# Performance work log

Measured on AMD Instinct MI355X. Metric: run time of the kernel, lower is better.

The kernel has to match this reference:

```python
import jax, jax.numpy as jnp
import numpy as np

K_CLS, M_PROTO, C = 19, 10, 720
EPS_SK, SK_ITERS = 0.05, 3  # standard distributed_sinkhorn defaults (SwAV/ProtoSeg)


def _layernorm(x, g, b, eps=1e-5):
    mu = jnp.mean(x, axis=-1, keepdims=True)
    var = jnp.var(x, axis=-1, keepdims=True)
    return (x - mu) * jax.lax.rsqrt(var + eps) * g + b


def _l2n(x):
    return x / jnp.clip(jnp.linalg.norm(x, axis=-1, keepdims=True), 1e-12, None)


def _masked_sinkhorn(scores, mask):
    # scores: [K, N, M] per-class similarity; mask: [K, N] (1.0 where gt_seg == class k)
    # Faithful to distributed_sinkhorn(init_q) run per class, vectorized over classes
    # with masking instead of data-dependent boolean gather (jit-safe).
    L = jnp.exp(scores / EPS_SK) * mask[..., None]                     # [K, N, M]
    L = L / jnp.clip(jnp.sum(L, axis=(1, 2), keepdims=True), 1e-12, None)
    n = jnp.sum(mask, axis=1)[:, None, None]                           # pixels per class [K,1,1]
    n_safe = jnp.maximum(n, 1.0)

    def body(L, _):
        # normalize each prototype row (sum over pixels), then divide by M
        L = L / jnp.clip(jnp.sum(L, axis=1, keepdims=True), 1e-12, None) / M_PROTO
        # normalize each pixel column (sum over prototypes), then divide by n
        L = L / jnp.clip(jnp.sum(L, axis=2, keepdims=True), 1e-12, None) / n_safe
        L = L * mask[..., None]
        return L, None

    L, _ = jax.lax.scan(body, L, None, length=SK_ITERS)
    return L * n_safe                                                  # [K, N, M]


def setup_inputs() -> dict:
    key = jax.random.key(0)
    k1, k2, k3 = jax.random.split(key, 3)
    N = 4 * 128 * 128  # batch 4, 512x512 crop at HRNet output stride 4
    return {
        "x": jax.random.normal(k1, (N, C), jnp.float32),
        "gt_seg": jax.random.randint(k2, (N,), 0, K_CLS),
        "feat_gamma": jnp.ones((C,), jnp.float32),
        "feat_beta": jnp.zeros((C,), jnp.float32),
        "prototypes": jax.random.normal(k3, (K_CLS, M_PROTO, C), jnp.float32) * 0.02,
    }


def reference(x, gt_seg, feat_gamma, feat_beta, prototypes):
    # similarity_compute (cosine branch)
    xn = _l2n(_layernorm(x, feat_gamma, feat_beta))                    # [N, C]
    protos = _l2n(prototypes)                                          # [K, M, C]
    sim_mat = jnp.einsum('nd,kmd->nmk', xn, protos)                    # [N, M, K]

    # prototype_learning
    s = jnp.max(sim_mat, axis=1)                                       # amax over prototypes -> [N, K]
    pred_seg = jnp.argmax(s, axis=-1)                                  # [N]
    scores = jnp.transpose(sim_mat, (2, 0, 1))                         # [K, N, M]
    mask = jnp.transpose(jax.nn.one_hot(gt_seg, K_CLS, dtype=sim_mat.dtype))  # [K, N]
    q = _masked_sinkhorn(scores, mask)                                 # [K, N, M]
    return sim_mat, q, pred_seg
```

## Files before the change

### kernel.cpp

```cpp
#include <hip/hip_runtime.h>
#include <stdint.h>

#define N_PIX    65536
#define C_DIM    720
#define K_CLS    19
#define M_PROTO  10
#define NPROTO   190
#define CPAD     768
#define OFF_Q    12451840
#define OFF_PRED 24903680

typedef _Float16 half8 __attribute__((ext_vector_type(8)));
typedef float    f32x4 __attribute__((ext_vector_type(4)));

#define WS_E       0u
#define WS_G2      768u
#define WS_G3      1536u
#define WS_CNT     2304u
#define WS_TIECNT  2432u
#define WS_V       2560u
#define WS_PSCALE  4096u
#define WS_EPIX    1052672u
#define WS_U       3674112u
#define WS_TIELIST 3936256u
#define WS_PF16    4198400u
#define WS_PF32    4493312u

__global__ void zero_acc(float* ws) {
    if (threadIdx.x < 640) ws[threadIdx.x] = 0.f;
}

__global__ void proto_prep(const float* __restrict__ protos,
                           _Float16* __restrict__ pf16,
                           float* __restrict__ pf32) {
    int p = blockIdx.x;
    int tid = threadIdx.x;
    if (p >= NPROTO) {
        for (int c = tid; c < CPAD; c += 256) pf16[(size_t)p * CPAD + c] = (_Float16)0.f;
        return;
    }
    __shared__ float red[256];
    const float* row = protos + (size_t)p * C_DIM;
    float ss = 0.f;
    for (int c = tid; c < C_DIM; c += 256) { float v = row[c]; ss += v * v; }
    red[tid] = ss;
    __syncthreads();
    for (int s = 128; s > 0; s >>= 1) {
        if (tid < s) red[tid] += red[tid + s];
        __syncthreads();
    }
    float invn = 1.f / fmaxf(sqrtf(red[0]), 1e-12f);
    for (int c = tid; c < CPAD; c += 256) {
        float v = (c < C_DIM) ? row[c] * invn : 0.f;
        pf16[(size_t)p * CPAD + c] = (_Float16)v;
        if (c < C_DIM) pf32[(size_t)p * C_DIM + c] = v;
    }
}

__global__ void stats_kernel(const float* __restrict__ x,
                             const float* __restrict__ gamma,
                             const float* __restrict__ beta,
                             float4* __restrict__ pscale) {
    int wave = threadIdx.x >> 6, lane = threadIdx.x & 63;
    int n = blockIdx.x * 4 + wave;
    const float* row = x + (size_t)n * C_DIM;
    float a[8];
    #pragma unroll
    for (int t = 0; t < 8; ++t) a[t] = 0.f;
    #pragma unroll
    for (int j = 0; j < 12; ++j) {
        int i = lane + 64 * j;
        if (i < C_DIM) {
            float v = row[i], g = gamma[i], b = beta[i];
            float g2 = g * g;
            a[0] += v;          a[1] += v * v;
            a[2] += v * g2;     a[3] += v * v * g2;
            a[4] += v * g * b;  a[5] += g2;
            a[6] += g * b;      a[7] += b * b;
        }
    }
    #pragma unroll
    for (int m = 1; m < 64; m <<= 1) {
        #pragma unroll
        for (int t = 0; t < 8; ++t) a[t] += __shfl_xor(a[t], m);
    }
    if (lane == 0) {
        float mu   = a[0] * (1.f / 720.f);
        float var  = a[1] * (1.f / 720.f) - mu * mu;
        float rsig = rsqrtf(var + 1e-5f);
        float ny2  = rsig * rsig * (a[3] - 2.f * mu * a[2] + mu * mu * a[5])
                   + 2.f * rsig * (a[4] - mu * a[6]) + a[7];
        float rn   = 1.f / fmaxf(sqrtf(fmaxf(ny2, 0.f)), 1e-12f);
        float pp   = rsig * rn;
        pscale[n]  = make_float4(pp, -pp * mu, rn, 0.f);
    }
}

__global__ __launch_bounds__(256) void gemm_sim(
        const float*  __restrict__ x,
        const float4* __restrict__ pscale,
        const float*  __restrict__ gamma,
        const float*  __restrict__ beta,
        const _Float16* __restrict__ pf16,
        const int*    __restrict__ gt_seg,
        float* __restrict__ out_sim,
        float* __restrict__ out_pred,
        float* __restrict__ epix,
        float* __restrict__ E,
        float* __restrict__ cnt,
        int*   __restrict__ tiecnt,
        int*   __restrict__ tielist) {
    __shared__ __align__(16) char smem[36864];
    _Float16* xs = (_Float16*)smem;
    _Float16* ps = (_Float16*)(smem + 9216);

    int tid = threadIdx.x;
    int wave = tid >> 6, lane = tid & 63;
    int lane15 = lane & 15, quad = lane >> 4;
    int n0 = blockIdx.x * 64;

    f32x4 acc[12];
    #pragma unroll
    for (int ct = 0; ct < 12; ++ct)
        acc[ct] = (f32x4){0.f, 0.f, 0.f, 0.f};

    #pragma unroll 1
    for (int ch = 0; ch < 12; ++ch) {
        __syncthreads();
        int kb4 = ch * 16;
        #pragma unroll
        for (int i = 0; i < 4; ++i) {
            int idx = tid + 256 * i;
            int r = idx >> 4, c4 = idx & 15;
            int gc4 = kb4 + c4;
            float4 xv = make_float4(0.f, 0.f, 0.f, 0.f);
            float4 gv = xv, bv = xv;
            if (gc4 < 180) {
                xv = *(const float4*)(x + (size_t)(n0 + r) * C_DIM + gc4 * 4);
                gv = *(const float4*)(gamma + gc4 * 4);
                bv = *(const float4*)(beta + gc4 * 4);
            }
            float4 sc = pscale[n0 + r];
            union { _Float16 h[4]; uint2 u; } cv;
            cv.h[0] = (_Float16)((sc.x * xv.x + sc.y) * gv.x + sc.z * bv.x);
            cv.h[1] = (_Float16)((sc.x * xv.y + sc.y) * gv.y + sc.z * bv.y);
            cv.h[2] = (_Float16)((sc.x * xv.z + sc.y) * gv.z + sc.z * bv.z);
            cv.h[3] = (_Float16)((sc.x * xv.w + sc.y) * gv.w + sc.z * bv.w);
            *reinterpret_cast<uint2*>(&xs[r * 72 + c4 * 4]) = cv.u;
        }
        #pragma unroll
        for (int i = 0; i < 6; ++i) {
            int idx = tid + 256 * i;
            int r = idx >> 3, c8 = idx & 7;
            int4 v = *(const int4*)(pf16 + (size_t)r * CPAD + ch * 64 + c8 * 8);
            *reinterpret_cast<int4*>(&ps[r * 72 + c8 * 8]) = v;
        }
        __syncthreads();
        #pragma unroll
        for (int ks = 0; ks < 2; ++ks) {
            int col = ks * 32 + quad * 8;
            half8 a0 = *reinterpret_cast<const half8*>(&xs[(wave * 16 + lane15) * 72 + col]);
            half8 b[12];
            #pragma unroll
            for (int ct = 0; ct < 12; ++ct)
                b[ct] = *reinterpret_cast<const half8*>(&ps[(ct * 16 + lane15) * 72 + col]);
            #pragma unroll
            for (int ct = 0; ct < 12; ++ct)
                acc[ct] = __builtin_amdgcn_mfma_f32_16x16x32_f16(a0, b[ct], acc[ct], 0, 0, 0);
        }
    }

    __syncthreads();
    float* fsm   = (float*)smem;
    float* ebuf  = fsm + wave * 1600;
    float* smaxw = fsm + 6400 + wave * 152;
    float* Eks   = fsm + 7008;
    float* hists = fsm + 7200;
    if (tid < 212) fsm[7008 + tid] = 0.f;
    __syncthreads();

    #pragma unroll
    for (int h = 0; h < 2; ++h) {
        if ((quad >> 1) == h) {
            int prow = (quad - 2 * h) * 4;
            #pragma unroll
            for (int ct = 0; ct < 12; ++ct) {
                int proto = ct * 16 + lane15;
                if (proto < NPROTO) {
                    int kc = proto / 10;
                    int m = proto - kc * 10;
                    int obase = m * 19 + kc;
                    #pragma unroll
                    for (int r = 0; r < 4; ++r)
                        ebuf[(prow + r) * 200 + obase] = acc[ct][r];
                }
            }
        }
        __syncthreads();
        #pragma unroll
        for (int p = 0; p < 8; ++p) {
            int pixel = n0 + wave * 16 + 8 * h + p;
            #pragma unroll
            for (int j = 0; j < 3; ++j) {
                int col = lane + 64 * j;
                if (col < NPROTO)
                    out_sim[(size_t)pixel * 190 + col] = ebuf[p * 200 + col];
            }
        }
        #pragma unroll
        for (int t = lane; t < 152; t += 64) {
            int p = t / 19, k = t - p * 19;
            const float* row = ebuf + p * 200;
            float mx = row[k];
            #pragma unroll
            for (int m = 1; m < 10; ++m) mx = fmaxf(mx, row[m * 19 + k]);
            smaxw[t] = mx;
        }
        __syncthreads();
        if (lane < 8) {
            int p = lane;
            int pixel = n0 + wave * 16 + 8 * h + p;
            float best = smaxw[p * 19], second = -1e30f;
            int bk = 0;
            #pragma unroll
            for (int k = 1; k < 19; ++k) {
                float v = smaxw[p * 19 + k];
                if (v > best) { second = best; best = v; bk = k; }
                else if (v > second) second = v;
            }
            out_pred[pixel] = (float)bk;
            if (best - second < 3e-4f) {
                int pos = atomicAdd(tiecnt, 1);
                if (pos < N_PIX) tielist[pos] = pixel;
            }
            int g = gt_seg[pixel];
            atomicAdd(&hists[g], 1.f);
            const float* row = ebuf + p * 200;
            #pragma unroll
            for (int m = 0; m < 10; ++m) {
                float ev = __expf(row[m * 19 + g] * 20.f);
                epix[(size_t)pixel * 10 + m] = ev;
                atomicAdd(&Eks[g * 10 + m], ev);
            }
        }
        __syncthreads();
    }
    if (tid < 190) atomicAdd(&E[tid], Eks[tid]);
    if (tid < 19)  atomicAdd(&cnt[tid], hists[tid]);
}

__global__ void tiefix(const float* __restrict__ x,
                       const float4* __restrict__ pscale,
                       const float* __restrict__ gamma,
                       const float* __restrict__ beta,
                       const float* __restrict__ pf32,
                       const int* __restrict__ tiecnt,
                       const int* __restrict__ tielist,
                       float* __restrict__ out_pred) {
    __shared__ float xrow[720];
    __shared__ double sd[190];
    int count = *tiecnt;
    if (count > N_PIX) count = N_PIX;
    int wave = threadIdx.x >> 6, lane = threadIdx.x & 63;
    for (int it = blockIdx.x; it < count; it += gridDim.x) {
        int n = tielist[it];
        float4 sc = pscale[n];
        for (int c = threadIdx.x; c < 720; c += 256)
            xrow[c] = (sc.x * x[(size_t)n * 720 + c] + sc.y) * gamma[c] + sc.z * beta[c];
        __syncthreads();
        for (int p = wave; p < NPROTO; p += 4) {
            const float* pr = pf32 + (size_t)p * 720;
            double a = 0.0;
            for (int j = 0; j < 12; ++j) {
                int i = lane + 64 * j;
                if (i < 720) a += (double)xrow[i] * (double)pr[i];
            }
            #pragma unroll
            for (int m = 1; m < 64; m <<= 1) a += __shfl_xor(a, m);
            if (lane == 0) sd[p] = a;
        }
        __syncthreads();
        if (threadIdx.x == 0) {
            double best = -1e300;
            int bk = 0;
            for (int k = 0; k < 19; ++k) {
                double sk = -1e300;
                for (int m = 0; m < 10; ++m) sk = fmax(sk, sd[k * 10 + m]);
                if (sk > best) { best = sk; bk = k; }
            }
            out_pred[n] = (float)bk;
        }
        __syncthreads();
    }
}

__global__ void v1k(const float* __restrict__ E, float* __restrict__ v) {
    __shared__ float Es[192];
    int t = threadIdx.x;
    if (t < 192) Es[t] = (t < 190) ? E[t] : 0.f;
    __syncthreads();
    if (t < 190) {
        int k = t / 10;
        float S = 0.f;
        #pragma unroll
        for (int m = 0; m < 10; ++m) S += Es[k * 10 + m];
        float v0 = 1.f / fmaxf(S, 1e-12f);
        float r = v0 * Es[t];
        v[t] = v0 / (fmaxf(r, 1e-12f) * 10.f);
    }
}

__global__ void v23k(float* __restrict__ v, const float* __restrict__ G) {
    int t = threadIdx.x;
    if (t < 190) {
        float r = v[t] * G[t];
        v[t] = v[t] / (fmaxf(r, 1e-12f) * 10.f);
    }
}

__global__ void pk(const float* __restrict__ epix,
                   const int* __restrict__ gt_seg,
                   const float* __restrict__ v,
                   const float* __restrict__ cnt,
                   const float* __restrict__ uin,
                   float* __restrict__ uout,
                   float* __restrict__ G) {
    __shared__ float vs[190];
    __shared__ float cs[19];
    __shared__ float Ga[190];
    int tid = threadIdx.x;
    if (tid < 190) { vs[tid] = v[tid]; Ga[tid] = 0.f; }
    if (tid < 19) cs[tid] = cnt[tid];
    __syncthreads();
    int n = blockIdx.x * 256 + tid;
    int g = gt_seg[n];
    float ns = fmaxf(cs[g], 1.f);
    const float* e = epix + (size_t)n * 10;
    float ev[10];
    float dot = 0.f;
    #pragma unroll
    for (int m = 0; m < 10; ++m) { ev[m] = e[m]; dot += ev[m] * vs[g * 10 + m]; }
    float up = uin ? uin[n] : 1.f;
    float c = up * dot;
    float u = up / (fmaxf(c, 1e-12f) * ns);
    uout[n] = u;
    #pragma unroll
    for (int m = 0; m < 10; ++m) atomicAdd(&Ga[g * 10 + m], ev[m] * u);
    __syncthreads();
    if (tid < 190) atomicAdd(&G[tid], Ga[tid]);
}

__global__ void p3k(const float* __restrict__ epix,
                    const int* __restrict__ gt_seg,
                    const float* __restrict__ v,
                    const float* __restrict__ cnt,
                    const float* __restrict__ uin,
                    float* __restrict__ qout) {
    __shared__ float vs[190];
    __shared__ float cs[19];
    int tid = threadIdx.x;
    if (tid < 190) vs[tid] = v[tid];
    if (tid < 19) cs[tid] = cnt[tid];
    __syncthreads();
    int n = blockIdx.x * 256 + tid;
    int g = gt_seg[n];
    float ns = fmaxf(cs[g], 1.f);
    const float* e = epix + (size_t)n * 10;
    float ev[10];
    float dot = 0.f;
    #pragma unroll
    for (int m = 0; m < 10; ++m) { ev[m] = e[m]; dot += ev[m] * vs[g * 10 + m]; }
    float up = uin[n];
    float c = up * dot;
    float u3 = up / (fmaxf(c, 1e-12f) * ns);
    float2 qv[5];
    #pragma unroll
    for (int j = 0; j < 5; ++j) {
        qv[j].x = ev[2 * j] * u3 * vs[g * 10 + 2 * j] * ns;
        qv[j].y = ev[2 * j + 1] * u3 * vs[g * 10 + 2 * j + 1] * ns;
    }
    const float2 z2 = make_float2(0.f, 0.f);
    for (int k = 0; k < 19; ++k) {
        float2* dst = reinterpret_cast<float2*>(qout + (size_t)k * 655360 + (size_t)n * 10);
        if (k == g) {
            #pragma unroll
            for (int j = 0; j < 5; ++j) dst[j] = qv[j];
        } else {
            #pragma unroll
            for (int j = 0; j < 5; ++j) dst[j] = z2;
        }
    }
}

extern "C" void kernel_launch(void* const* d_in, const int* in_sizes, int n_in,
                              void* d_out, int out_size, void* d_ws, size_t ws_size,
                              hipStream_t stream) {
    const float* x      = (const float*)d_in[0];
    const int*   gt     = (const int*)d_in[1];
    const float* gamma  = (const float*)d_in[2];
    const float* beta   = (const float*)d_in[3];
    const float* protos = (const float*)d_in[4];
    float* out = (float*)d_out;
    char* ws = (char*)d_ws;

    float*  E       = (float*)(ws + WS_E);
    float*  G2      = (float*)(ws + WS_G2);
    float*  G3      = (float*)(ws + WS_G3);
    float*  cnt     = (float*)(ws + WS_CNT);
    int*    tiecnt  = (int*)(ws + WS_TIECNT);
    float*  v       = (float*)(ws + WS_V);
    float4* pscale  = (float4*)(ws + WS_PSCALE);
    float*  epix    = (float*)(ws + WS_EPIX);
    float*  u       = (float*)(ws + WS_U);
    int*    tielist = (int*)(ws + WS_TIELIST);
    _Float16* pf16  = (_Float16*)(ws + WS_PF16);
    float*  pf32    = (float*)(ws + WS_PF32);

    zero_acc<<<1, 1024, 0, stream>>>((float*)ws);
    proto_prep<<<192, 256, 0, stream>>>(protos, pf16, pf32);
    stats_kernel<<<16384, 256, 0, stream>>>(x, gamma, beta, pscale);
    gemm_sim<<<1024, 256, 0, stream>>>(x, pscale, gamma, beta, pf16, gt,
                                       out, out + OFF_PRED, epix, E, cnt, tiecnt, tielist);
    tiefix<<<1024, 256, 0, stream>>>(x, pscale, gamma, beta, pf32, tiecnt, tielist, out + OFF_PRED);
    v1k<<<1, 256, 0, stream>>>(E, v);
    pk<<<256, 256, 0, stream>>>(epix, gt, v, cnt, nullptr, u, G2);
    v23k<<<1, 256, 0, stream>>>(v, G2);
    pk<<<256, 256, 0, stream>>>(epix, gt, v, cnt, u, u, G3);
    v23k<<<1, 256, 0, stream>>>(v, G3);
    p3k<<<256, 256, 0, stream>>>(epix, gt, v, cnt, u, out + OFF_Q);
}
```

Before: 494.0 us.

## Precompute fp16 normalized features, async-load swizzled tiles, fuse Sinkhorn scalar kernels

The stats kernel now writes the layernormed, L2-normalized features as fp16 into an XOR-swizzled, padded workspace buffer. The GEMM then streams both operands straight into LDS with global_load_lds, replacing the fp32 loads and per-chunk conversion. This removes the fp32 re-read and the transform arithmetic from the GEMM and avoids LDS bank conflicts without padding, at the cost of an extra fp16 write and read of the activations. Separately, the tiny v1k/v23k launches are folded into the per-pixel Sinkhorn kernels, which recompute the prototype scale vectors redundantly in every block, removing three serial launches.

```diff
diff --git a/kernel.cpp b/kernel.cpp
--- a/kernel.cpp
+++ b/kernel.cpp
@@ -11,6 +11,7 @@
 #define OFF_PRED 24903680
 
 typedef _Float16 half8 __attribute__((ext_vector_type(8)));
+typedef _Float16 h4    __attribute__((ext_vector_type(4)));
 typedef float    f32x4 __attribute__((ext_vector_type(4)));
 
 #define WS_E       0u
@@ -18,13 +19,19 @@
 #define WS_G3      1536u
 #define WS_CNT     2304u
 #define WS_TIECNT  2432u
-#define WS_V       2560u
 #define WS_PSCALE  4096u
 #define WS_EPIX    1052672u
 #define WS_U       3674112u
 #define WS_TIELIST 3936256u
 #define WS_PF16    4198400u
 #define WS_PF32    4493312u
+#define WS_XH      5046272u
+
+__device__ __forceinline__ void async16(const void* g, void* l) {
+    __builtin_amdgcn_global_load_lds(
+        (const __attribute__((address_space(1))) unsigned int*)g,
+        (__attribute__((address_space(3))) unsigned int*)l, 16, 0, 0);
+}
 
 __global__ void zero_acc(float* ws) {
     if (threadIdx.x < 640) ws[threadIdx.x] = 0.f;
@@ -50,57 +57,76 @@
         __syncthreads();
     }
     float invn = 1.f / fmaxf(sqrtf(red[0]), 1e-12f);
+    int e8 = p & 7;
     for (int c = tid; c < CPAD; c += 256) {
         float v = (c < C_DIM) ? row[c] * invn : 0.f;
-        pf16[(size_t)p * CPAD + c] = (_Float16)v;
+        int sw = (((c >> 3) ^ e8) << 3) | (c & 7);
+        pf16[(size_t)p * CPAD + sw] = (_Float16)v;
         if (c < C_DIM) pf32[(size_t)p * C_DIM + c] = v;
     }
 }
 
-__global__ void stats_kernel(const float* __restrict__ x,
-                             const float* __restrict__ gamma,
-                             const float* __restrict__ beta,
-                             float4* __restrict__ pscale) {
+__global__ __launch_bounds__(256) void stats_xh(const float* __restrict__ x,
+                                                const float* __restrict__ gamma,
+                                                const float* __restrict__ beta,
+                                                float4* __restrict__ pscale,
+                                                _Float16* __restrict__ xh) {
     int wave = threadIdx.x >> 6, lane = threadIdx.x & 63;
     int n = blockIdx.x * 4 + wave;
-    const float* row = x + (size_t)n * C_DIM;
+    const float4* row4 = (const float4*)(x + (size_t)n * C_DIM);
+    const float4* g4 = (const float4*)gamma;
+    const float4* b4 = (const float4*)beta;
+
     float a[8];
     #pragma unroll
     for (int t = 0; t < 8; ++t) a[t] = 0.f;
-    #pragma unroll
-    for (int j = 0; j < 12; ++j) {
-        int i = lane + 64 * j;
-        if (i < C_DIM) {
-            float v = row[i], g = gamma[i], b = beta[i];
-            float g2 = g * g;
-            a[0] += v;          a[1] += v * v;
-            a[2] += v * g2;     a[3] += v * v * g2;
-            a[4] += v * g * b;  a[5] += g2;
-            a[6] += g * b;      a[7] += b * b;
-        }
+    float4 xv[3], gv[3], bv[3];
+    #pragma unroll
+    for (int j = 0; j < 3; ++j) {
+        int f = lane + 64 * j;
+        float4 xvv = make_float4(0.f, 0.f, 0.f, 0.f), gvv = xvv, bvv = xvv;
+        if (f < 180) { xvv = row4[f]; gvv = g4[f]; bvv = b4[f]; }
+        xv[j] = xvv; gv[j] = gvv; bv[j] = bvv;
+        #define ACC1(v, g, b) { float g2 = (g)*(g); a[0] += (v); a[1] += (v)*(v); \
+            a[2] += (v)*g2; a[3] += (v)*(v)*g2; a[4] += (v)*(g)*(b); a[5] += g2; \
+            a[6] += (g)*(b); a[7] += (b)*(b); }
+        ACC1(xvv.x, gvv.x, bvv.x); ACC1(xvv.y, gvv.y, bvv.y);
+        ACC1(xvv.z, gvv.z, bvv.z); ACC1(xvv.w, gvv.w, bvv.w);
+        #undef ACC1
     }
     #pragma unroll
     for (int m = 1; m < 64; m <<= 1) {
         #pragma unroll
         for (int t = 0; t < 8; ++t) a[t] += __shfl_xor(a[t], m);
     }
-    if (lane == 0) {
-        float mu   = a[0] * (1.f / 720.f);
-        float var  = a[1] * (1.f / 720.f) - mu * mu;
-        float rsig = rsqrtf(var + 1e-5f);
-        float ny2  = rsig * rsig * (a[3] - 2.f * mu * a[2] + mu * mu * a[5])
-                   + 2.f * rsig * (a[4] - mu * a[6]) + a[7];
-        float rn   = 1.f / fmaxf(sqrtf(fmaxf(ny2, 0.f)), 1e-12f);
-        float pp   = rsig * rn;
-        pscale[n]  = make_float4(pp, -pp * mu, rn, 0.f);
+    float mu   = a[0] * (1.f / 720.f);
+    float var  = a[1] * (1.f / 720.f) - mu * mu;
+    float rsig = rsqrtf(var + 1e-5f);
+    float ny2  = rsig * rsig * (a[3] - 2.f * mu * a[2] + mu * mu * a[5])
+               + 2.f * rsig * (a[4] - mu * a[6]) + a[7];
+    float rn   = 1.f / fmaxf(sqrtf(fmaxf(ny2, 0.f)), 1e-12f);
+    float pp   = rsig * rn;
+    float qq   = -pp * mu;
+    if (lane == 0) pscale[n] = make_float4(pp, qq, rn, 0.f);
+
+    int e8 = n & 7;
+    _Float16* orow = xh + (size_t)n * CPAD;
+    #pragma unroll
+    for (int j = 0; j < 3; ++j) {
+        int f = lane + 64 * j;
+        float4 xvv = xv[j], gvv = gv[j], bvv = bv[j];
+        h4 o;
+        o.x = (_Float16)((pp * xvv.x + qq) * gvv.x + rn * bvv.x);
+        o.y = (_Float16)((pp * xvv.y + qq) * gvv.y + rn * bvv.y);
+        o.z = (_Float16)((pp * xvv.z + qq) * gvv.z + rn * bvv.z);
+        o.w = (_Float16)((pp * xvv.w + qq) * gvv.w + rn * bvv.w);
+        int off = ((((f >> 1) ^ e8) << 3) | ((f & 1) << 2));
+        *reinterpret_cast<h4*>(orow + off) = o;
     }
 }
 
 __global__ __launch_bounds__(256) void gemm_sim(
-        const float*  __restrict__ x,
-        const float4* __restrict__ pscale,
-        const float*  __restrict__ gamma,
-        const float*  __restrict__ beta,
+        const _Float16* __restrict__ xh,
         const _Float16* __restrict__ pf16,
         const int*    __restrict__ gt_seg,
         float* __restrict__ out_sim,
@@ -110,14 +136,15 @@
         float* __restrict__ cnt,
         int*   __restrict__ tiecnt,
         int*   __restrict__ tielist) {
-    __shared__ __align__(16) char smem[36864];
+    __shared__ __align__(16) char smem[32768];
     _Float16* xs = (_Float16*)smem;
-    _Float16* ps = (_Float16*)(smem + 9216);
+    _Float16* ps = (_Float16*)(smem + 8192);
 
     int tid = threadIdx.x;
     int wave = tid >> 6, lane = tid & 63;
     int lane15 = lane & 15, quad = lane >> 4;
     int n0 = blockIdx.x * 64;
+    int rsub = lane >> 3, csub = (lane & 7) << 3;
 
     f32x4 acc[12];
     #pragma unroll
@@ -127,43 +154,28 @@
     #pragma unroll 1
     for (int ch = 0; ch < 12; ++ch) {
         __syncthreads();
-        int kb4 = ch * 16;
-        #pragma unroll
-        for (int i = 0; i < 4; ++i) {
-            int idx = tid + 256 * i;
-            int r = idx >> 4, c4 = idx & 15;
-            int gc4 = kb4 + c4;
-            float4 xv = make_float4(0.f, 0.f, 0.f, 0.f);
-            float4 gv = xv, bv = xv;
-            if (gc4 < 180) {
-                xv = *(const float4*)(x + (size_t)(n0 + r) * C_DIM + gc4 * 4);
-                gv = *(const float4*)(gamma + gc4 * 4);
-                bv = *(const float4*)(beta + gc4 * 4);
-            }
-            float4 sc = pscale[n0 + r];
-            union { _Float16 h[4]; uint2 u; } cv;
-            cv.h[0] = (_Float16)((sc.x * xv.x + sc.y) * gv.x + sc.z * bv.x);
-            cv.h[1] = (_Float16)((sc.x * xv.y + sc.y) * gv.y + sc.z * bv.y);
-            cv.h[2] = (_Float16)((sc.x * xv.z + sc.y) * gv.z + sc.z * bv.z);
-            cv.h[3] = (_Float16)((sc.x * xv.w + sc.y) * gv.w + sc.z * bv.w);
-            *reinterpret_cast<uint2*>(&xs[r * 72 + c4 * 4]) = cv.u;
+        #pragma unroll
+        for (int i = 0; i < 2; ++i) {
+            int r0 = wave * 16 + i * 8;
+            const _Float16* g = xh + (size_t)(n0 + r0 + rsub) * CPAD + ch * 64 + csub;
+            async16(g, xs + r0 * 64);
         }
         #pragma unroll
         for (int i = 0; i < 6; ++i) {
-            int idx = tid + 256 * i;
-            int r = idx >> 3, c8 = idx & 7;
-            int4 v = *(const int4*)(pf16 + (size_t)r * CPAD + ch * 64 + c8 * 8);
-            *reinterpret_cast<int4*>(&ps[r * 72 + c8 * 8]) = v;
-        }
-        __syncthreads();
+            int r0 = wave * 48 + i * 8;
+            const _Float16* g = pf16 + (size_t)(r0 + rsub) * CPAD + ch * 64 + csub;
+            async16(g, ps + r0 * 64);
+        }
+        __syncthreads();
+        int e8 = lane15 & 7;
         #pragma unroll
         for (int ks = 0; ks < 2; ++ks) {
-            int col = ks * 32 + quad * 8;
-            half8 a0 = *reinterpret_cast<const half8*>(&xs[(wave * 16 + lane15) * 72 + col]);
+            int so = (((ks * 4 + quad) ^ e8) << 3);
+            half8 a0 = *reinterpret_cast<const half8*>(xs + (wave * 16 + lane15) * 64 + so);
             half8 b[12];
             #pragma unroll
             for (int ct = 0; ct < 12; ++ct)
-                b[ct] = *reinterpret_cast<const half8*>(&ps[(ct * 16 + lane15) * 72 + col]);
+                b[ct] = *reinterpret_cast<const half8*>(ps + (ct * 16 + lane15) * 64 + so);
             #pragma unroll
             for (int ct = 0; ct < 12; ++ct)
                 acc[ct] = __builtin_amdgcn_mfma_f32_16x16x32_f16(a0, b[ct], acc[ct], 0, 0, 0);
@@ -294,43 +306,32 @@
     }
 }
 
-__global__ void v1k(const float* __restrict__ E, float* __restrict__ v) {
-    __shared__ float Es[192];
-    int t = threadIdx.x;
-    if (t < 192) Es[t] = (t < 190) ? E[t] : 0.f;
-    __syncthreads();
-    if (t < 190) {
-        int k = t / 10;
-        float S = 0.f;
-        #pragma unroll
-        for (int m = 0; m < 10; ++m) S += Es[k * 10 + m];
-        float v0 = 1.f / fmaxf(S, 1e-12f);
-        float r = v0 * Es[t];
-        v[t] = v0 / (fmaxf(r, 1e-12f) * 10.f);
-    }
-}
-
-__global__ void v23k(float* __restrict__ v, const float* __restrict__ G) {
-    int t = threadIdx.x;
-    if (t < 190) {
-        float r = v[t] * G[t];
-        v[t] = v[t] / (fmaxf(r, 1e-12f) * 10.f);
-    }
-}
-
-__global__ void pk(const float* __restrict__ epix,
-                   const int* __restrict__ gt_seg,
-                   const float* __restrict__ v,
-                   const float* __restrict__ cnt,
-                   const float* __restrict__ uin,
-                   float* __restrict__ uout,
-                   float* __restrict__ G) {
+__global__ void pk_fused(const float* __restrict__ epix,
+                         const int* __restrict__ gt_seg,
+                         const float* __restrict__ E,
+                         const float* __restrict__ Gprev,
+                         const float* __restrict__ cnt,
+                         const float* __restrict__ uin,
+                         float* __restrict__ uout,
+                         float* __restrict__ Gout) {
+    __shared__ float Es[190];
     __shared__ float vs[190];
     __shared__ float cs[19];
     __shared__ float Ga[190];
     int tid = threadIdx.x;
-    if (tid < 190) { vs[tid] = v[tid]; Ga[tid] = 0.f; }
+    if (tid < 190) { Es[tid] = E[tid]; Ga[tid] = 0.f; }
     if (tid < 19) cs[tid] = cnt[tid];
+    __syncthreads();
+    if (tid < 190) {
+        int k = tid / 10;
+        float S = 0.f;
+        #pragma unroll
+        for (int m = 0; m < 10; ++m) S += Es[k * 10 + m];
+        float v0 = 1.f / fmaxf(S, 1e-12f);
+        float vv = v0 / (fmaxf(v0 * Es[tid], 1e-12f) * 10.f);
+        if (Gprev) vv = vv / (fmaxf(vv * Gprev[tid], 1e-12f) * 10.f);
+        vs[tid] = vv;
+    }
     __syncthreads();
     int n = blockIdx.x * 256 + tid;
     int g = gt_seg[n];
@@ -342,25 +343,40 @@
     for (int m = 0; m < 10; ++m) { ev[m] = e[m]; dot += ev[m] * vs[g * 10 + m]; }
     float up = uin ? uin[n] : 1.f;
     float c = up * dot;
-    float u = up / (fmaxf(c, 1e-12f) * ns);
-    uout[n] = u;
-    #pragma unroll
-    for (int m = 0; m < 10; ++m) atomicAdd(&Ga[g * 10 + m], ev[m] * u);
-    __syncthreads();
-    if (tid < 190) atomicAdd(&G[tid], Ga[tid]);
-}
-
-__global__ void p3k(const float* __restrict__ epix,
-                    const int* __restrict__ gt_seg,
-                    const float* __restrict__ v,
-                    const float* __restrict__ cnt,
-                    const float* __restrict__ uin,
-                    float* __restrict__ qout) {
+    float uu = up / (fmaxf(c, 1e-12f) * ns);
+    uout[n] = uu;
+    #pragma unroll
+    for (int m = 0; m < 10; ++m) atomicAdd(&Ga[g * 10 + m], ev[m] * uu);
+    __syncthreads();
+    if (tid < 190) atomicAdd(&Gout[tid], Ga[tid]);
+}
+
+__global__ void p3k_fused(const float* __restrict__ epix,
+                          const int* __restrict__ gt_seg,
+                          const float* __restrict__ E,
+                          const float* __restrict__ G2,
+                          const float* __restrict__ G3,
+                          const float* __restrict__ cnt,
+                          const float* __restrict__ uin,
+                          float* __restrict__ qout) {
+    __shared__ float Es[190];
     __shared__ float vs[190];
     __shared__ float cs[19];
     int tid = threadIdx.x;
-    if (tid < 190) vs[tid] = v[tid];
+    if (tid < 190) Es[tid] = E[tid];
     if (tid < 19) cs[tid] = cnt[tid];
+    __syncthreads();
+    if (tid < 190) {
+        int k = tid / 10;
+        float S = 0.f;
+        #pragma unroll
+        for (int m = 0; m < 10; ++m) S += Es[k * 10 + m];
+        float v0 = 1.f / fmaxf(S, 1e-12f);
+        float vv = v0 / (fmaxf(v0 * Es[tid], 1e-12f) * 10.f);
+        vv = vv / (fmaxf(vv * G2[tid], 1e-12f) * 10.f);
+        vv = vv / (fmaxf(vv * G3[tid], 1e-12f) * 10.f);
+        vs[tid] = vv;
+    }
     __syncthreads();
     int n = blockIdx.x * 256 + tid;
     int g = gt_seg[n];
@@ -408,24 +424,21 @@
     float*  G3      = (float*)(ws + WS_G3);
     float*  cnt     = (float*)(ws + WS_CNT);
     int*    tiecnt  = (int*)(ws + WS_TIECNT);
-    float*  v       = (float*)(ws + WS_V);
     float4* pscale  = (float4*)(ws + WS_PSCALE);
     float*  epix    = (float*)(ws + WS_EPIX);
     float*  u       = (float*)(ws + WS_U);
     int*    tielist = (int*)(ws + WS_TIELIST);
     _Float16* pf16  = (_Float16*)(ws + WS_PF16);
     float*  pf32    = (float*)(ws + WS_PF32);
+    _Float16* xh    = (_Float16*)(ws + WS_XH);
 
     zero_acc<<<1, 1024, 0, stream>>>((float*)ws);
     proto_prep<<<192, 256, 0, stream>>>(protos, pf16, pf32);
-    stats_kernel<<<16384, 256, 0, stream>>>(x, gamma, beta, pscale);
-    gemm_sim<<<1024, 256, 0, stream>>>(x, pscale, gamma, beta, pf16, gt,
+    stats_xh<<<16384, 256, 0, stream>>>(x, gamma, beta, pscale, xh);
+    gemm_sim<<<1024, 256, 0, stream>>>(xh, pf16, gt,
                                        out, out + OFF_PRED, epix, E, cnt, tiecnt, tielist);
     tiefix<<<1024, 256, 0, stream>>>(x, pscale, gamma, beta, pf32, tiecnt, tielist, out + OFF_PRED);
-    v1k<<<1, 256, 0, stream>>>(E, v);
-    pk<<<256, 256, 0, stream>>>(epix, gt, v, cnt, nullptr, u, G2);
-    v23k<<<1, 256, 0, stream>>>(v, G2);
-    pk<<<256, 256, 0, stream>>>(epix, gt, v, cnt, u, u, G3);
-    v23k<<<1, 256, 0, stream>>>(v, G3);
-    p3k<<<256, 256, 0, stream>>>(epix, gt, v, cnt, u, out + OFF_Q);
-}
+    pk_fused<<<256, 256, 0, stream>>>(epix, gt, E, nullptr, cnt, nullptr, u, G2);
+    pk_fused<<<256, 256, 0, stream>>>(epix, gt, E, G2, cnt, u, u, G3);
+    p3k_fused<<<256, 256, 0, stream>>>(epix, gt, E, G2, G3, cnt, u, out + OFF_Q);
+}
```

Result: no change. 502.7 us (+1.8%).
